# Kernel tuning notes

Measured on AMD Instinct MI355X. Metric: run time of the kernel, lower is better.

## Reference

```python
import jax, jax.numpy as jnp
import numpy as np

N_FRAGMENTS = 4_000_000
D_EMBED = 64
CELL_N = 1000
GENE_N = 1000


def setup_inputs() -> dict:
    key = jax.random.key(0)
    k1, k2 = jax.random.split(key)
    embedding = jax.random.normal(k1, (N_FRAGMENTS, D_EMBED), dtype=jnp.float32)
    fragment_cellxgene_ix = jnp.sort(
        jax.random.randint(k2, (N_FRAGMENTS,), 0, CELL_N * GENE_N, dtype=jnp.int64)
    )
    return {
        "embedding": embedding,
        "fragment_cellxgene_ix": fragment_cellxgene_ix,
        "cell_n": CELL_N,
        "gene_n": GENE_N,
    }


def reference(embedding, fragment_cellxgene_ix, cell_n, gene_n):
    # segment_sum_coo over sorted indices -> [cell_n*gene_n, d]
    cellxgene_embedding = jax.ops.segment_sum(
        embedding,
        fragment_cellxgene_ix,
        num_segments=cell_n * gene_n,
        indices_are_sorted=True,
    )
    # free reshape to [cell_n, gene_n, d]
    return cellxgene_embedding.reshape((cell_n, gene_n, embedding.shape[-1]))
```

## Files before the change

### kernel.cpp

```cpp
#include <hip/hip_runtime.h>
#include <hip/hip_bf16.h>


#define SEGS_PER_WAVE 64
#define D_EMBED 64
#define BATCH 16

__device__ inline int lower_bound(const int* __restrict__ idx, int n, int v) {
    int lo = 0, hi = n;
    while (lo < hi) {
        int mid = (lo + hi) >> 1;
        if (idx[mid] < v) lo = mid + 1; else hi = mid;
    }
    return lo;
}

__global__ __launch_bounds__(256) void seg_sum_kernel(
        const float* __restrict__ emb,
        const int*   __restrict__ idx,
        float*       __restrict__ out,
        int n_frag, int n_seg) {
    const int gtid = blockIdx.x * blockDim.x + threadIdx.x;
    const int wave = gtid >> 6;
    const int lane = threadIdx.x & 63;

    const int s0 = wave * SEGS_PER_WAVE;
    if (s0 >= n_seg) return;
    const int s1 = min(s0 + SEGS_PER_WAVE, n_seg);

    int       f  = lower_bound(idx, n_frag, s0);
    const int f1 = lower_bound(idx, n_frag, s1);

    int   cur = -1;
    int   nxt = s0;
    float acc = 0.0f;

    float vA[BATCH], vB[BATCH];
    int   mA = 0, mB = 0;

    auto LOAD_A = [&](long fb) {
        mA = idx[fb + (lane & (BATCH - 1))];
        const float* base = emb + fb * D_EMBED + lane;
#pragma unroll
        for (int j = 0; j < BATCH; ++j) vA[j] = base[j * D_EMBED];
    };
    auto LOAD_B = [&](long fb) {
        mB = idx[fb + (lane & (BATCH - 1))];
        const float* base = emb + fb * D_EMBED + lane;
#pragma unroll
        for (int j = 0; j < BATCH; ++j) vB[j] = base[j * D_EMBED];
    };
    auto WALK = [&](const float* v, int mseg) {
#pragma unroll
        for (int j = 0; j < BATCH; ++j) {
            int s = __builtin_amdgcn_readlane(mseg, j);
            if (s != cur) {
                if (cur >= 0) { out[(long)cur * D_EMBED + lane] = acc; nxt = cur + 1; }
                for (int z = nxt; z < s; ++z)
                    out[(long)z * D_EMBED + lane] = 0.0f;
                cur = s; nxt = s; acc = 0.0f;
            }
            acc += v[j];
        }
    };

    const int nfull = (f1 - f) >> 4;
    long fcur = f;
    int  b = 0;
    if (nfull > 0) LOAD_A(fcur);
    while (b < nfull) {
        if (b + 1 < nfull) LOAD_B(fcur + BATCH);
        WALK(vA, mA);
        fcur += BATCH; ++b;
        if (b >= nfull) break;
        if (b + 1 < nfull) LOAD_A(fcur + BATCH);
        WALK(vB, mB);
        fcur += BATCH; ++b;
    }

    for (long ff = (long)f + (long)nfull * BATCH; ff < f1; ++ff) {
        int   s = idx[ff];
        float v = emb[ff * D_EMBED + lane];
        if (s != cur) {
            if (cur >= 0) { out[(long)cur * D_EMBED + lane] = acc; nxt = cur + 1; }
            for (int z = nxt; z < s; ++z)
                out[(long)z * D_EMBED + lane] = 0.0f;
            cur = s; nxt = s; acc = 0.0f;
        }
        acc += v;
    }

    if (cur >= 0) { out[(long)cur * D_EMBED + lane] = acc; nxt = cur + 1; }
    for (int z = nxt; z < s1; ++z)
        out[(long)z * D_EMBED + lane] = 0.0f;
}

extern "C" void kernel_launch(void* const* d_in, const int* in_sizes, int n_in,
                              void* d_out, int out_size, void* d_ws, size_t ws_size,
                              hipStream_t stream) {
    const float* emb = (const float*)d_in[0];
    const int*   idx = (const int*)d_in[1];
    float*       out = (float*)d_out;

    const int n_frag = in_sizes[0] / D_EMBED;
    const int n_seg  = out_size / D_EMBED;

    const int n_waves  = (n_seg + SEGS_PER_WAVE - 1) / SEGS_PER_WAVE;
    const int block    = 256;
    const int waves_pb = block / 64;
    const int grid     = (n_waves + waves_pb - 1) / waves_pb;

    seg_sum_kernel<<<grid, block, 0, stream>>>(emb, idx, out, n_frag, n_seg);
}
```

Baseline: 287.5 us.

## Vectorize segment-sum loads to float4 with quarter-wave fragment split and shuffle reduce

Each lane now loads float4 chunks, so a wave reads four fragments per instruction instead of one row, and each quarter-wave accumulates its own fragment. At each segment boundary the four partial accumulators are combined with xor shuffles and 16 lanes write a float4 row using nontemporal stores. The goal is fewer, wider memory instructions and less cache pollution on the streaming traffic. In exchange, every boundary now costs 8 shuffles, and with roughly 4 fragments per nonempty segment that overhead may be significant. Zero-fill stores are also narrowed to 16 lanes.

```diff
diff --git a/kernel.cpp b/kernel.cpp
--- a/kernel.cpp
+++ b/kernel.cpp
@@ -5,6 +5,8 @@
 #define SEGS_PER_WAVE 64
 #define D_EMBED 64
 #define BATCH 16
+
+typedef float f32x4 __attribute__((ext_vector_type(4)));
 
 __device__ inline int lower_bound(const int* __restrict__ idx, int n, int v) {
     int lo = 0, hi = n;
@@ -23,6 +25,8 @@
     const int gtid = blockIdx.x * blockDim.x + threadIdx.x;
     const int wave = gtid >> 6;
     const int lane = threadIdx.x & 63;
+    const int q    = lane >> 4;
+    const int r    = lane & 15;
 
     const int s0 = wave * SEGS_PER_WAVE;
     if (s0 >= n_seg) return;
@@ -31,36 +35,56 @@
     int       f  = lower_bound(idx, n_frag, s0);
     const int f1 = lower_bound(idx, n_frag, s1);
 
+    const f32x4 ZERO4 = {0.f, 0.f, 0.f, 0.f};
     int   cur = -1;
     int   nxt = s0;
-    float acc = 0.0f;
+    f32x4 acc = ZERO4;
 
-    float vA[BATCH], vB[BATCH];
+    auto BOUNDARY = [&](int s) {
+        if (cur >= 0) {
+            f32x4 t = acc;
+            t[0] += __shfl_xor(t[0], 16); t[1] += __shfl_xor(t[1], 16);
+            t[2] += __shfl_xor(t[2], 16); t[3] += __shfl_xor(t[3], 16);
+            t[0] += __shfl_xor(t[0], 32); t[1] += __shfl_xor(t[1], 32);
+            t[2] += __shfl_xor(t[2], 32); t[3] += __shfl_xor(t[3], 32);
+            if (lane < 16)
+                __builtin_nontemporal_store(t, (f32x4*)(out + (long)cur * D_EMBED) + r);
+            nxt = cur + 1;
+        }
+        for (int z = nxt; z < s; ++z)
+            if (lane < 16)
+                __builtin_nontemporal_store(ZERO4, (f32x4*)(out + (long)z * D_EMBED) + r);
+        cur = s; nxt = s; acc = ZERO4;
+    };
+
+    f32x4 a0, a1, a2, a3, b0, b1, b2, b3;
     int   mA = 0, mB = 0;
 
     auto LOAD_A = [&](long fb) {
-        mA = idx[fb + (lane & (BATCH - 1))];
-        const float* base = emb + fb * D_EMBED + lane;
-#pragma unroll
-        for (int j = 0; j < BATCH; ++j) vA[j] = base[j * D_EMBED];
+        mA = idx[fb + r];
+        const f32x4* bp = (const f32x4*)(emb + fb * D_EMBED) + lane;
+        a0 = __builtin_nontemporal_load(bp);
+        a1 = __builtin_nontemporal_load(bp + 64);
+        a2 = __builtin_nontemporal_load(bp + 128);
+        a3 = __builtin_nontemporal_load(bp + 192);
     };
     auto LOAD_B = [&](long fb) {
-        mB = idx[fb + (lane & (BATCH - 1))];
-        const float* base = emb + fb * D_EMBED + lane;
-#pragma unroll
-        for (int j = 0; j < BATCH; ++j) vB[j] = base[j * D_EMBED];
+        mB = idx[fb + r];
+        const f32x4* bp = (const f32x4*)(emb + fb * D_EMBED) + lane;
+        b0 = __builtin_nontemporal_load(bp);
+        b1 = __builtin_nontemporal_load(bp + 64);
+        b2 = __builtin_nontemporal_load(bp + 128);
+        b3 = __builtin_nontemporal_load(bp + 192);
     };
-    auto WALK = [&](const float* v, int mseg) {
+    auto WALK = [&](const f32x4& v0, const f32x4& v1, const f32x4& v2,
+                    const f32x4& v3, int mseg) {
 #pragma unroll
         for (int j = 0; j < BATCH; ++j) {
             int s = __builtin_amdgcn_readlane(mseg, j);
-            if (s != cur) {
-                if (cur >= 0) { out[(long)cur * D_EMBED + lane] = acc; nxt = cur + 1; }
-                for (int z = nxt; z < s; ++z)
-                    out[(long)z * D_EMBED + lane] = 0.0f;
-                cur = s; nxt = s; acc = 0.0f;
-            }
-            acc += v[j];
+            if (s != cur) BOUNDARY(s);
+            const f32x4 vj = (j >> 2) == 0 ? v0 : (j >> 2) == 1 ? v1
+                           : (j >> 2) == 2 ? v2 : v3;
+            if (q == (j & 3)) acc += vj;
         }
     };
 
@@ -70,29 +94,23 @@
     if (nfull > 0) LOAD_A(fcur);
     while (b < nfull) {
         if (b + 1 < nfull) LOAD_B(fcur + BATCH);
-        WALK(vA, mA);
+        WALK(a0, a1, a2, a3, mA);
         fcur += BATCH; ++b;
         if (b >= nfull) break;
         if (b + 1 < nfull) LOAD_A(fcur + BATCH);
-        WALK(vB, mB);
+        WALK(b0, b1, b2, b3, mB);
         fcur += BATCH; ++b;
     }
 
     for (long ff = (long)f + (long)nfull * BATCH; ff < f1; ++ff) {
-        int   s = idx[ff];
-        float v = emb[ff * D_EMBED + lane];
-        if (s != cur) {
-            if (cur >= 0) { out[(long)cur * D_EMBED + lane] = acc; nxt = cur + 1; }
-            for (int z = nxt; z < s; ++z)
-                out[(long)z * D_EMBED + lane] = 0.0f;
-            cur = s; nxt = s; acc = 0.0f;
-        }
-        acc += v;
+        int s = idx[ff];
+        f32x4 v = __builtin_nontemporal_load(
+            (const f32x4*)(emb + ff * D_EMBED) + r);
+        if (s != cur) BOUNDARY(s);
+        if (q == 0) acc += v;
     }
 
-    if (cur >= 0) { out[(long)cur * D_EMBED + lane] = acc; nxt = cur + 1; }
-    for (int z = nxt; z < s1; ++z)
-        out[(long)z * D_EMBED + lane] = 0.0f;
+    BOUNDARY(s1);
 }
 
 extern "C" void kernel_launch(void* const* d_in, const int* in_sizes, int n_in,
```

New measurement: 276.9 us. 3.7% less time.

## Stage segment outputs in LDS and stream them out with vector nontemporal stores

Applied to the files above, without the earlier changes.

Each wave now gets its own 64-thread block and writes segment sums and zero-fills into a 16KB LDS tile instead of scattering them straight to global memory. At the end it copies the tile out with contiguous 16-byte nontemporal stores. Embedding loads are also marked nontemporal. This aims to make the output-write path (256MB) fully coalesced and vectorised, but 16KB of LDS per single-wave block may limit how many waves fit on each CU and hurt latency hiding.

```diff
diff --git a/kernel.cpp b/kernel.cpp
--- a/kernel.cpp
+++ b/kernel.cpp
@@ -5,6 +5,8 @@
 #define SEGS_PER_WAVE 64
 #define D_EMBED 64
 #define BATCH 16
+
+typedef float f32x4 __attribute__((ext_vector_type(4)));
 
 __device__ inline int lower_bound(const int* __restrict__ idx, int n, int v) {
     int lo = 0, hi = n;
@@ -15,14 +17,15 @@
     return lo;
 }
 
-__global__ __launch_bounds__(256) void seg_sum_kernel(
+__global__ __launch_bounds__(64) void seg_sum_kernel(
         const float* __restrict__ emb,
         const int*   __restrict__ idx,
         float*       __restrict__ out,
         int n_frag, int n_seg) {
-    const int gtid = blockIdx.x * blockDim.x + threadIdx.x;
-    const int wave = gtid >> 6;
-    const int lane = threadIdx.x & 63;
+    __shared__ float tile[SEGS_PER_WAVE * D_EMBED];
+
+    const int wave = blockIdx.x;
+    const int lane = threadIdx.x;
 
     const int s0 = wave * SEGS_PER_WAVE;
     if (s0 >= n_seg) return;
@@ -35,6 +38,13 @@
     int   nxt = s0;
     float acc = 0.0f;
 
+    auto BOUNDARY = [&](int s) {
+        if (cur >= 0) { tile[(cur - s0) * D_EMBED + lane] = acc; nxt = cur + 1; }
+        for (int z = nxt; z < s; ++z)
+            tile[(z - s0) * D_EMBED + lane] = 0.0f;
+        cur = s; nxt = s; acc = 0.0f;
+    };
+
     float vA[BATCH], vB[BATCH];
     int   mA = 0, mB = 0;
 
@@ -42,24 +52,21 @@
         mA = idx[fb + (lane & (BATCH - 1))];
         const float* base = emb + fb * D_EMBED + lane;
 #pragma unroll
-        for (int j = 0; j < BATCH; ++j) vA[j] = base[j * D_EMBED];
+        for (int j = 0; j < BATCH; ++j)
+            vA[j] = __builtin_nontemporal_load(base + j * D_EMBED);
     };
     auto LOAD_B = [&](long fb) {
         mB = idx[fb + (lane & (BATCH - 1))];
         const float* base = emb + fb * D_EMBED + lane;
 #pragma unroll
-        for (int j = 0; j < BATCH; ++j) vB[j] = base[j * D_EMBED];
+        for (int j = 0; j < BATCH; ++j)
+            vB[j] = __builtin_nontemporal_load(base + j * D_EMBED);
     };
     auto WALK = [&](const float* v, int mseg) {
 #pragma unroll
         for (int j = 0; j < BATCH; ++j) {
             int s = __builtin_amdgcn_readlane(mseg, j);
-            if (s != cur) {
-                if (cur >= 0) { out[(long)cur * D_EMBED + lane] = acc; nxt = cur + 1; }
-                for (int z = nxt; z < s; ++z)
-                    out[(long)z * D_EMBED + lane] = 0.0f;
-                cur = s; nxt = s; acc = 0.0f;
-            }
+            if (s != cur) BOUNDARY(s);
             acc += v[j];
         }
     };
@@ -81,18 +88,18 @@
     for (long ff = (long)f + (long)nfull * BATCH; ff < f1; ++ff) {
         int   s = idx[ff];
         float v = emb[ff * D_EMBED + lane];
-        if (s != cur) {
-            if (cur >= 0) { out[(long)cur * D_EMBED + lane] = acc; nxt = cur + 1; }
-            for (int z = nxt; z < s; ++z)
-                out[(long)z * D_EMBED + lane] = 0.0f;
-            cur = s; nxt = s; acc = 0.0f;
-        }
+        if (s != cur) BOUNDARY(s);
         acc += v;
     }
 
-    if (cur >= 0) { out[(long)cur * D_EMBED + lane] = acc; nxt = cur + 1; }
-    for (int z = nxt; z < s1; ++z)
-        out[(long)z * D_EMBED + lane] = 0.0f;
+    BOUNDARY(s1);
+
+    const int nvec = (s1 - s0) * D_EMBED / 4;
+    const f32x4* tp = (const f32x4*)tile;
+    f32x4*       op = (f32x4*)(out + (long)s0 * D_EMBED);
+#pragma unroll 4
+    for (int i = lane; i < nvec; i += 64)
+        __builtin_nontemporal_store(tp[i], op + i);
 }
 
 extern "C" void kernel_launch(void* const* d_in, const int* in_sizes, int n_in,
@@ -105,10 +112,6 @@
     const int n_frag = in_sizes[0] / D_EMBED;
     const int n_seg  = out_size / D_EMBED;
 
-    const int n_waves  = (n_seg + SEGS_PER_WAVE - 1) / SEGS_PER_WAVE;
-    const int block    = 256;
-    const int waves_pb = block / 64;
-    const int grid     = (n_waves + waves_pb - 1) / waves_pb;
-
-    seg_sum_kernel<<<grid, block, 0, stream>>>(emb, idx, out, n_frag, n_seg);
+    const int n_waves = (n_seg + SEGS_PER_WAVE - 1) / SEGS_PER_WAVE;
+    seg_sum_kernel<<<n_waves, 64, 0, stream>>>(emb, idx, out, n_frag, n_seg);
 }
```

After: 232.6 us (median of 2 runs). -19.1%, faster.
